# Optimization experiments

Hardware: AMD Instinct MI355X
Metric: run time of the kernel (lower is better)

Reference implementation:

```python
import jax, jax.numpy as jnp
import numpy as np

NEG_SLOPE = 0.01  # nn.LeakyReLU default

N = 100000
E = 1600000
D_IN = 128
D_OUT = 128


def setup_inputs() -> dict:
    key = jax.random.key(0)
    ks = jax.random.split(key, 8)
    features = jax.random.normal(ks[0], (N, D_IN), dtype=jnp.float32)
    adj_rows = jax.random.randint(ks[1], (E,), 0, N, dtype=jnp.int64)
    adj_cols = jax.random.randint(ks[2], (E,), 0, N, dtype=jnp.int64)
    adj_vals = jax.random.uniform(ks[3], (E,), dtype=jnp.float32)
    s1 = 1.0 / np.sqrt(D_IN)
    W1 = jax.random.uniform(ks[4], (D_IN, D_OUT), jnp.float32, -s1, s1)
    b1 = jax.random.uniform(ks[5], (D_OUT,), jnp.float32, -s1, s1)
    W2 = jax.random.uniform(ks[6], (D_IN, D_OUT), jnp.float32, -s1, s1)
    b2 = jax.random.uniform(ks[7], (D_OUT,), jnp.float32, -s1, s1)
    return {"features": features, "adj_rows": adj_rows, "adj_cols": adj_cols,
            "adj_vals": adj_vals, "W1": W1, "b1": b1, "W2": W2, "b2": b2}


def reference(features, adj_rows, adj_cols, adj_vals, W1, b1, W2, b2):
    # h_neigh = adj @ features  (COO SpMM via gather + segment_sum)
    msgs = adj_vals[:, None] * features[adj_cols]          # [E, D_IN]
    h_neigh = jax.ops.segment_sum(msgs, adj_rows, num_segments=features.shape[0])
    term1 = (features + h_neigh) @ W1 + b1                 # W1(features + h_neigh)
    term2 = (features * h_neigh) @ W2 + b2                 # W2(features * h_neigh)
    pre = term1 + term2
    return jnp.where(pre >= 0, pre, NEG_SLOPE * pre)       # leaky_relu
```

## Files before the change

### kernel.cpp

```cpp
#include <hip/hip_runtime.h>

#define D 128
#define BM 64

typedef short short8 __attribute__((ext_vector_type(8)));
typedef unsigned short ushort8_t __attribute__((ext_vector_type(8)));
typedef float f32x4 __attribute__((ext_vector_type(4)));

__device__ __forceinline__ unsigned short f2bf(float x) {
    unsigned u = __float_as_uint(x);
    unsigned r = (u + 0x7fffu + ((u >> 16) & 1u)) >> 16;
    return (unsigned short)r;
}
__device__ __forceinline__ float bf2f(unsigned short u) {
    return __uint_as_float(((unsigned)u) << 16);
}

__global__ __launch_bounds__(256) void prep_kernel(
    const float4* __restrict__ feat4, ushort4* __restrict__ fbf4, int nf4,
    const float* __restrict__ W1, const float* __restrict__ W2,
    unsigned short* __restrict__ WT,
    const int* __restrict__ rows, int* __restrict__ bcnt,
    int E, int nb, int epb)
{
    __shared__ int cnt[1024];
    const int t = threadIdx.x;
    const int b = blockIdx.x;
    for (int i = t; i < nb; i += 256) cnt[i] = 0;
    __syncthreads();

    int e0 = b * epb;
    int e1 = e0 + epb; if (e1 > E) e1 = E;
    for (int e = e0 + t; e < e1; e += 256) atomicAdd(&cnt[rows[e] >> 7], 1);

    for (int i = b * 256 + t; i < nf4; i += 256 * 256) {
        float4 v = feat4[i];
        fbf4[i] = make_ushort4(f2bf(v.x), f2bf(v.y), f2bf(v.z), f2bf(v.w));
    }

    if (b < 128) {
        int idx = b * 256 + t;
        int c = idx & 127;
        int k = idx >> 7;
        float w = (k < 128) ? W1[k * 128 + c] : W2[(k - 128) * 128 + c];
        WT[c * 256 + k] = f2bf(w);
    }

    __syncthreads();
    for (int i = t; i < nb; i += 256)
        if (cnt[i]) atomicAdd(&bcnt[i], cnt[i]);
}

__global__ __launch_bounds__(256) void fconv_kernel(
    const float4* __restrict__ feat4, ushort4* __restrict__ fbf4, int total)
{
    int i = blockIdx.x * 256 + threadIdx.x;
    if (i < total) {
        float4 v = feat4[i];
        fbf4[i] = make_ushort4(f2bf(v.x), f2bf(v.y), f2bf(v.z), f2bf(v.w));
    }
}

__global__ __launch_bounds__(256) void wconv_kernel(
    const float* __restrict__ W1, const float* __restrict__ W2,
    unsigned short* __restrict__ WT)
{
    int idx = blockIdx.x * 256 + threadIdx.x;
    int c = idx & 127;
    int k = idx >> 7;
    float w = (k < 128) ? W1[k * 128 + c] : W2[(k - 128) * 128 + c];
    WT[c * 256 + k] = f2bf(w);
}

__global__ __launch_bounds__(1024) void bucket_scan_kernel(
    const int* __restrict__ bcnt, int* __restrict__ bstart,
    int* __restrict__ bcur, int nb, int E)
{
    __shared__ int wsum[16];
    int tid = threadIdx.x, lane = tid & 63, wid = tid >> 6;
    int x = (tid < nb) ? bcnt[tid] : 0;
    int v = x;
    #pragma unroll
    for (int off = 1; off < 64; off <<= 1) {
        int y = __shfl_up(v, off, 64);
        if (lane >= off) v += y;
    }
    if (lane == 63) wsum[wid] = v;
    __syncthreads();
    if (wid == 0 && lane < 16) {
        int s = wsum[lane];
        #pragma unroll
        for (int off = 1; off < 16; off <<= 1) {
            int y = __shfl_up(s, off, 64);
            if (lane >= off) s += y;
        }
        wsum[lane] = s;
    }
    __syncthreads();
    int wexcl = wid ? wsum[wid - 1] : 0;
    int excl = wexcl + v - x;
    if (tid < nb) { bstart[tid] = excl; bcur[tid] = excl; }
    if (tid == 0) bstart[nb] = E;
}

__global__ __launch_bounds__(256) void bucket_scatter_kernel(
    const int* __restrict__ rows, const int* __restrict__ cols,
    const float* __restrict__ vals, int* __restrict__ bcur,
    uint2* __restrict__ bsedge, int E, int nb)
{
    __shared__ int cnt[1024];
    __shared__ int base[1024];
    int t = threadIdx.x;
    int e0 = blockIdx.x * 4096;
    for (int i = t; i < nb; i += 256) cnt[i] = 0;
    __syncthreads();
    #pragma unroll
    for (int q = 0; q < 16; ++q) {
        int e = e0 + t + q * 256;
        if (e < E) atomicAdd(&cnt[rows[e] >> 7], 1);
    }
    __syncthreads();
    for (int i = t; i < nb; i += 256) {
        int c = cnt[i];
        if (c) { base[i] = atomicAdd(&bcur[i], c); cnt[i] = 0; }
    }
    __syncthreads();
    #pragma unroll
    for (int q = 0; q < 16; ++q) {
        int e = e0 + t + q * 256;
        if (e < E) {
            int r = rows[e];
            int b = r >> 7;
            int pos = base[b] + atomicAdd(&cnt[b], 1);
            bsedge[pos] = make_uint2(((unsigned)(r & 127) << 17) | (unsigned)cols[e],
                                     __float_as_uint(vals[e]));
        }
    }
}

__global__ __launch_bounds__(256) void bucket_sort_kernel(
    const uint2* __restrict__ bsedge,
    const int* __restrict__ bstart,
    uint2* __restrict__ sedge,
    int* __restrict__ row_start,
    int N, int E)
{
    __shared__ int cnt[128];
    __shared__ int base[128];
    const int b = blockIdx.x;
    const int t = threadIdx.x;
    const int s = bstart[b], e = bstart[b + 1];
    if (t < 128) cnt[t] = 0;
    __syncthreads();
    for (int j = s + t; j < e; j += 256)
        atomicAdd(&cnt[bsedge[j].x >> 17], 1);
    __syncthreads();
    if (t < 64) {
        int c0 = cnt[2 * t], c1 = cnt[2 * t + 1];
        int pair = c0 + c1;
        int v = pair;
        #pragma unroll
        for (int off = 1; off < 64; off <<= 1) {
            int y = __shfl_up(v, off, 64);
            if (t >= off) v += y;
        }
        int excl = v - pair;
        base[2 * t]     = excl;
        base[2 * t + 1] = excl + c0;
        cnt[2 * t] = 0;
        cnt[2 * t + 1] = 0;
    }
    __syncthreads();
    const int r0 = b << 7;
    if (t < 128 && r0 + t < N) row_start[r0 + t] = s + base[t];
    if (b == 0 && t == 0) row_start[N] = E;
    for (int j = s + t; j < e; j += 256) {
        uint2 ed = bsedge[j];
        int rl = ed.x >> 17;
        int p = atomicAdd(&cnt[rl], 1);
        sedge[s + base[rl] + p] = make_uint2(ed.x & 0x1FFFFu, ed.y);
    }
}

__global__ __launch_bounds__(256) void spmm_ab_kernel(
    const ushort8_t* __restrict__ fbf8,
    const int* __restrict__ row_start,
    const uint2* __restrict__ sedge,
    unsigned char* __restrict__ ambf, int N)
{
    int t = blockIdx.x * 256 + threadIdx.x;
    int row  = t >> 5;
    int half = (t >> 4) & 1;
    int l    = t & 15;
    if (row >= N) return;

    int s = row_start[row];
    int e = row_start[row + 1];
    int mid = s + ((e - s + 1) >> 1);
    int j0 = half ? mid : s;
    int j1 = half ? e : mid;

    float acc[8] = {};
    int j = j0;
    for (; j + 3 < j1; j += 4) {
        uint2 e0 = sedge[j],     e1 = sedge[j + 1];
        uint2 e2 = sedge[j + 2], e3 = sedge[j + 3];
        ushort8_t f0 = fbf8[(size_t)e0.x * 16 + l];
        ushort8_t f1 = fbf8[(size_t)e1.x * 16 + l];
        ushort8_t f2 = fbf8[(size_t)e2.x * 16 + l];
        ushort8_t f3 = fbf8[(size_t)e3.x * 16 + l];
        float v0 = __uint_as_float(e0.y), v1 = __uint_as_float(e1.y);
        float v2 = __uint_as_float(e2.y), v3 = __uint_as_float(e3.y);
        #pragma unroll
        for (int q = 0; q < 8; ++q) {
            acc[q] = fmaf(v0, bf2f(f0[q]), acc[q]);
            acc[q] = fmaf(v1, bf2f(f1[q]), acc[q]);
            acc[q] = fmaf(v2, bf2f(f2[q]), acc[q]);
            acc[q] = fmaf(v3, bf2f(f3[q]), acc[q]);
        }
    }
    for (; j < j1; ++j) {
        uint2 e0 = sedge[j];
        float v = __uint_as_float(e0.y);
        ushort8_t f0 = fbf8[(size_t)e0.x * 16 + l];
        #pragma unroll
        for (int q = 0; q < 8; ++q) acc[q] = fmaf(v, bf2f(f0[q]), acc[q]);
    }

    #pragma unroll
    for (int q = 0; q < 8; ++q)
        acc[q] += __shfl_xor(acc[q], 16, 64);

    if (half == 0) {
        ushort8_t fown = fbf8[(size_t)row * 16 + l];
        ushort8_t av, mv;
        #pragma unroll
        for (int q = 0; q < 8; ++q) {
            float f = bf2f(fown[q]);
            av[q] = f2bf(f + acc[q]);
            mv[q] = f2bf(f * acc[q]);
        }
        int swz = (row & 7) << 4;
        unsigned char* rowp = ambf + (size_t)row * 512;
        *(ushort8_t*)(rowp + ((16 * l) ^ swz))       = av;
        *(ushort8_t*)(rowp + 256 + ((16 * l) ^ swz)) = mv;
    }
}

__global__ __launch_bounds__(256) void mfma_gemm2_kernel(
    const unsigned char* __restrict__ ambf,
    const unsigned short* __restrict__ WT,
    const float* __restrict__ b1, const float* __restrict__ b2,
    float* __restrict__ out, int N)
{
    __shared__ __align__(16) unsigned char am_raw[64 * 512];

    const int tid = threadIdx.x;
    const int block0 = blockIdx.x * BM;

    const short8* src = (const short8*)(ambf + (size_t)block0 * 512);
    short8* dst = (short8*)am_raw;
    #pragma unroll
    for (int it = 0; it < 8; ++it) {
        int idx = tid + it * 256;
        dst[idx] = src[idx];
    }
    __syncthreads();

    const int lane = tid & 63;
    const int w    = tid >> 6;
    const int wr   = w >> 1;
    const int wc   = w & 1;
    const int l15  = lane & 15;
    const int lk   = lane >> 4;
    const int rswz = (l15 & 7) << 4;

    f32x4 acc[2][4] = {};

    const char* WTc = (const char*)WT;
    const unsigned char* arow0 = am_raw + (wr * 32 + l15) * 512;
    const unsigned char* arow1 = arow0 + 16 * 512;

    #pragma unroll
    for (int ks = 0; ks < 8; ++ks) {
        int kbyte = ks * 64 + lk * 16;
        int akoff = kbyte ^ rswz;
        short8 a0 = *(const short8*)(arow0 + akoff);
        short8 a1 = *(const short8*)(arow1 + akoff);
        short8 bfr[4];
        #pragma unroll
        for (int nc = 0; nc < 4; ++nc) {
            int col = wc * 64 + nc * 16 + l15;
            bfr[nc] = *(const short8*)(WTc + col * 512 + kbyte);
        }
        #pragma unroll
        for (int nc = 0; nc < 4; ++nc) {
            acc[0][nc] = __builtin_amdgcn_mfma_f32_16x16x32_bf16(a0, bfr[nc], acc[0][nc], 0, 0, 0);
            acc[1][nc] = __builtin_amdgcn_mfma_f32_16x16x32_bf16(a1, bfr[nc], acc[1][nc], 0, 0, 0);
        }
    }

    #pragma unroll
    for (int nc = 0; nc < 4; ++nc) {
        int col = wc * 64 + nc * 16 + l15;
        float bias = b1[col] + b2[col];
        #pragma unroll
        for (int mr = 0; mr < 2; ++mr) {
            int rbase = block0 + wr * 32 + mr * 16 + lk * 4;
            #pragma unroll
            for (int r = 0; r < 4; ++r) {
                int row = rbase + r;
                if (row < N) {
                    float v = acc[mr][nc][r] + bias;
                    out[row * 128 + col] = (v >= 0.f) ? v : 0.01f * v;
                }
            }
        }
    }
}

__global__ __launch_bounds__(256) void hist_kernel(
    const int* __restrict__ rows, int* __restrict__ counts, int E)
{
    int e = blockIdx.x * 256 + threadIdx.x;
    if (e < E) atomicAdd(&counts[rows[e]], 1);
}

__global__ __launch_bounds__(256) void scan_pass1(
    const int* __restrict__ counts, int* __restrict__ btot, int N)
{
    int tid = threadIdx.x;
    int i = blockIdx.x * 1024 + tid * 4;
    int s = 0;
    if (i + 3 < N) {
        int4 v = *(const int4*)(counts + i);
        s = v.x + v.y + v.z + v.w;
    } else {
        for (int q = 0; q < 4; ++q) if (i + q < N) s += counts[i + q];
    }
    #pragma unroll
    for (int off = 32; off >= 1; off >>= 1) s += __shfl_down(s, off, 64);
    __shared__ int ws[4];
    if ((tid & 63) == 0) ws[tid >> 6] = s;
    __syncthreads();
    if (tid == 0) btot[blockIdx.x] = ws[0] + ws[1] + ws[2] + ws[3];
}

__global__ __launch_bounds__(1024) void scan_pass2(
    const int* __restrict__ btot, int* __restrict__ boff, int nb)
{
    __shared__ int wsum[16];
    int tid = threadIdx.x, lane = tid & 63, wid = tid >> 6;
    int x = (tid < nb) ? btot[tid] : 0;
    int v = x;
    #pragma unroll
    for (int off = 1; off < 64; off <<= 1) {
        int y = __shfl_up(v, off, 64);
        if (lane >= off) v += y;
    }
    if (lane == 63) wsum[wid] = v;
    __syncthreads();
    if (wid == 0 && lane < 16) {
        int s = wsum[lane];
        #pragma unroll
        for (int off = 1; off < 16; off <<= 1) {
            int y = __shfl_up(s, off, 64);
            if (lane >= off) s += y;
        }
        wsum[lane] = s;
    }
    __syncthreads();
    int wexcl = wid ? wsum[wid - 1] : 0;
    if (tid < nb) boff[tid] = wexcl + v - x;
}

__global__ __launch_bounds__(256) void scan_pass3(
    int* __restrict__ row_start, int* __restrict__ cursor,
    const int* __restrict__ boff, int N, int E)
{
    int tid = threadIdx.x;
    int base = blockIdx.x * 1024 + tid * 4;
    int c0 = 0, c1 = 0, c2 = 0, c3 = 0;
    if (base + 3 < N) {
        int4 v = *(const int4*)(row_start + base);
        c0 = v.x; c1 = v.y; c2 = v.z; c3 = v.w;
    } else {
        if (base + 0 < N) c0 = row_start[base + 0];
        if (base + 1 < N) c1 = row_start[base + 1];
        if (base + 2 < N) c2 = row_start[base + 2];
        if (base + 3 < N) c3 = row_start[base + 3];
    }
    int s0 = c0, s1 = s0 + c1, s2 = s1 + c2, s3 = s2 + c3;
    int lane = tid & 63, wid = tid >> 6;
    int v = s3;
    #pragma unroll
    for (int off = 1; off < 64; off <<= 1) {
        int y = __shfl_up(v, off, 64);
        if (lane >= off) v += y;
    }
    __shared__ int ws[4];
    if (lane == 63) ws[wid] = v;
    __syncthreads();
    int wexcl = 0;
    for (int q = 0; q < wid; ++q) wexcl += ws[q];
    int texcl = wexcl + (v - s3) + boff[blockIdx.x];
    int e0 = texcl, e1 = texcl + s0, e2 = texcl + s1, e3 = texcl + s2;
    if (base + 0 < N) { row_start[base + 0] = e0; cursor[base + 0] = e0; }
    if (base + 1 < N) { row_start[base + 1] = e1; cursor[base + 1] = e1; }
    if (base + 2 < N) { row_start[base + 2] = e2; cursor[base + 2] = e2; }
    if (base + 3 < N) { row_start[base + 3] = e3; cursor[base + 3] = e3; }
    if (blockIdx.x == 0 && tid == 0) row_start[N] = E;
}

__global__ __launch_bounds__(256) void scatter_sort_kernel(
    const int* __restrict__ rows, const int* __restrict__ cols,
    const float* __restrict__ vals, int* __restrict__ cursor,
    uint2* __restrict__ sedge, int E)
{
    int e = blockIdx.x * 256 + threadIdx.x;
    if (e < E) {
        int r = rows[e];
        int p = atomicAdd(&cursor[r], 1);
        sedge[p] = make_uint2((unsigned)cols[e], __float_as_uint(vals[e]));
    }
}

__global__ __launch_bounds__(256) void spmm_kernel(
    const float2* __restrict__ feat2,
    const int* __restrict__ row_start,
    const uint2* __restrict__ sedge,
    float2* __restrict__ h2, int N)
{
    int gw = (blockIdx.x * 256 + threadIdx.x) >> 6;
    int lane = threadIdx.x & 63;
    if (gw >= N) return;
    int s = row_start[gw];
    int e = row_start[gw + 1];
    float2 acc = make_float2(0.f, 0.f);
    int j = s;
    for (; j + 1 < e; j += 2) {
        uint2 e0 = sedge[j], e1 = sedge[j + 1];
        float v0 = __uint_as_float(e0.y), v1 = __uint_as_float(e1.y);
        float2 f0 = feat2[(size_t)e0.x * 64 + lane];
        float2 f1 = feat2[(size_t)e1.x * 64 + lane];
        acc.x = fmaf(v0, f0.x, acc.x);
        acc.y = fmaf(v0, f0.y, acc.y);
        acc.x = fmaf(v1, f1.x, acc.x);
        acc.y = fmaf(v1, f1.y, acc.y);
    }
    if (j < e) {
        uint2 e0 = sedge[j];
        float v = __uint_as_float(e0.y);
        float2 f = feat2[(size_t)e0.x * 64 + lane];
        acc.x = fmaf(v, f.x, acc.x);
        acc.y = fmaf(v, f.y, acc.y);
    }
    h2[(size_t)gw * 64 + lane] = acc;
}

__global__ __launch_bounds__(256) void mfma_gemm_kernel(
    const float4* __restrict__ feat4, const float4* __restrict__ h4,
    const unsigned short* __restrict__ WT,
    const float* __restrict__ b1, const float* __restrict__ b2,
    float* __restrict__ out, int N)
{
    __shared__ __align__(16) unsigned char am_raw[64 * 512];
    const int tid = threadIdx.x;
    const int block0 = blockIdx.x * BM;
    #pragma unroll
    for (int it = 0; it < 8; ++it) {
        int idx  = tid + it * 256;
        int node = idx >> 5;
        int p    = idx & 31;
        int g    = block0 + node;
        float4 fv = make_float4(0.f, 0.f, 0.f, 0.f);
        float4 hv = make_float4(0.f, 0.f, 0.f, 0.f);
        if (g < N) { fv = feat4[g * 32 + p]; hv = h4[g * 32 + p]; }
        ushort4 av = make_ushort4(f2bf(fv.x + hv.x), f2bf(fv.y + hv.y),
                                  f2bf(fv.z + hv.z), f2bf(fv.w + hv.w));
        ushort4 mv = make_ushort4(f2bf(fv.x * hv.x), f2bf(fv.y * hv.y),
                                  f2bf(fv.z * hv.z), f2bf(fv.w * hv.w));
        int swz = (node & 7) << 4;
        *(ushort4*)(am_raw + node * 512 + ((p * 8) ^ swz))       = av;
        *(ushort4*)(am_raw + node * 512 + ((256 + p * 8) ^ swz)) = mv;
    }
    __syncthreads();
    const int lane = tid & 63;
    const int w    = tid >> 6;
    const int wr   = w >> 1;
    const int wc   = w & 1;
    const int l15  = lane & 15;
    const int lk   = lane >> 4;
    const int rswz = (l15 & 7) << 4;
    f32x4 acc[2][4] = {};
    const char* WTc = (const char*)WT;
    const unsigned char* arow0 = am_raw + (wr * 32 + l15) * 512;
    const unsigned char* arow1 = arow0 + 16 * 512;
    #pragma unroll
    for (int ks = 0; ks < 8; ++ks) {
        int kbyte = ks * 64 + lk * 16;
        int akoff = kbyte ^ rswz;
        short8 a0 = *(const short8*)(arow0 + akoff);
        short8 a1 = *(const short8*)(arow1 + akoff);
        short8 bfr[4];
        #pragma unroll
        for (int nc = 0; nc < 4; ++nc) {
            int col = wc * 64 + nc * 16 + l15;
            bfr[nc] = *(const short8*)(WTc + col * 512 + kbyte);
        }
        #pragma unroll
        for (int nc = 0; nc < 4; ++nc) {
            acc[0][nc] = __builtin_amdgcn_mfma_f32_16x16x32_bf16(a0, bfr[nc], acc[0][nc], 0, 0, 0);
            acc[1][nc] = __builtin_amdgcn_mfma_f32_16x16x32_bf16(a1, bfr[nc], acc[1][nc], 0, 0, 0);
        }
    }
    #pragma unroll
    for (int nc = 0; nc < 4; ++nc) {
        int col = wc * 64 + nc * 16 + l15;
        float bias = b1[col] + b2[col];
        #pragma unroll
        for (int mr = 0; mr < 2; ++mr) {
            int rbase = block0 + wr * 32 + mr * 16 + lk * 4;
            #pragma unroll
            for (int r = 0; r < 4; ++r) {
                int row = rbase + r;
                if (row < N) {
                    float v = acc[mr][nc][r] + bias;
                    out[row * 128 + col] = (v >= 0.f) ? v : 0.01f * v;
                }
            }
        }
    }
}

__global__ __launch_bounds__(256) void edge_scatter_kernel(
    const float4* __restrict__ feat4, const int* __restrict__ rows,
    const int* __restrict__ cols, const float* __restrict__ vals,
    float* __restrict__ h, int E)
{
    int idx = blockIdx.x * 256 + threadIdx.x;
    if (idx >= E * 32) return;
    int e = idx >> 5;
    int p = idx & 31;
    int r = rows[e];
    int c = cols[e];
    float v = vals[e];
    float4 f = feat4[c * 32 + p];
    float* hr = h + (long long)r * D + p * 4;
    unsafeAtomicAdd(hr + 0, v * f.x);
    unsafeAtomicAdd(hr + 1, v * f.y);
    unsafeAtomicAdd(hr + 2, v * f.z);
    unsafeAtomicAdd(hr + 3, v * f.w);
}

__global__ __launch_bounds__(256) void fused_gemm_kernel(
    const float* __restrict__ feat, const float* __restrict__ h,
    const float* __restrict__ W1, const float* __restrict__ b1,
    const float* __restrict__ W2, const float* __restrict__ b2,
    float* __restrict__ out, int N)
{
    __shared__ float a_lds[BM][D];
    __shared__ float m_lds[BM][D];
    const int tid = threadIdx.x;
    const int block0 = blockIdx.x * BM;
    const float4* feat4 = (const float4*)feat;
    const float4* h4    = (const float4*)h;
    #pragma unroll
    for (int it = 0; it < 8; ++it) {
        int idx  = tid + it * 256;
        int node = idx >> 5;
        int p    = idx & 31;
        int gnode = block0 + node;
        float4 fv = make_float4(0.f, 0.f, 0.f, 0.f);
        float4 hv = make_float4(0.f, 0.f, 0.f, 0.f);
        if (gnode < N) { fv = feat4[gnode * 32 + p]; hv = h4[gnode * 32 + p]; }
        float4 av = make_float4(fv.x + hv.x, fv.y + hv.y, fv.z + hv.z, fv.w + hv.w);
        float4 mv = make_float4(fv.x * hv.x, fv.y * hv.y, fv.z * hv.z, fv.w * hv.w);
        *(float4*)&a_lds[node][p * 4] = av;
        *(float4*)&m_lds[node][p * 4] = mv;
    }
    __syncthreads();
    const int c = tid & 31;
    const int g = tid >> 5;
    float acc[8][4] = {};
    const float4* W1v = (const float4*)W1;
    const float4* W2v = (const float4*)W2;
    for (int k = 0; k < D; ++k) {
        float4 w1 = W1v[k * 32 + c];
        float4 w2 = W2v[k * 32 + c];
        #pragma unroll
        for (int t = 0; t < 8; ++t) {
            float av = a_lds[g + 8 * t][k];
            float mv = m_lds[g + 8 * t][k];
            acc[t][0] = fmaf(av, w1.x, fmaf(mv, w2.x, acc[t][0]));
            acc[t][1] = fmaf(av, w1.y, fmaf(mv, w2.y, acc[t][1]));
            acc[t][2] = fmaf(av, w1.z, fmaf(mv, w2.z, acc[t][2]));
            acc[t][3] = fmaf(av, w1.w, fmaf(mv, w2.w, acc[t][3]));
        }
    }
    float4 bb1 = ((const float4*)b1)[c];
    float4 bb2 = ((const float4*)b2)[c];
    const float bx = bb1.x + bb2.x, by = bb1.y + bb2.y;
    const float bz = bb1.z + bb2.z, bw = bb1.w + bb2.w;
    #pragma unroll
    for (int t = 0; t < 8; ++t) {
        int gnode = block0 + g + 8 * t;
        if (gnode >= N) continue;
        float4 o;
        o.x = acc[t][0] + bx; o.y = acc[t][1] + by;
        o.z = acc[t][2] + bz; o.w = acc[t][3] + bw;
        o.x = (o.x >= 0.f) ? o.x : 0.01f * o.x;
        o.y = (o.y >= 0.f) ? o.y : 0.01f * o.y;
        o.z = (o.z >= 0.f) ? o.z : 0.01f * o.z;
        o.w = (o.w >= 0.f) ? o.w : 0.01f * o.w;
        ((float4*)out)[gnode * 32 + c] = o;
    }
}

extern "C" void kernel_launch(void* const* d_in, const int* in_sizes, int n_in,
                              void* d_out, int out_size, void* d_ws, size_t ws_size,
                              hipStream_t stream) {
    const float* feat = (const float*)d_in[0];
    const int*   rows = (const int*)d_in[1];
    const int*   cols = (const int*)d_in[2];
    const float* vals = (const float*)d_in[3];
    const float* W1   = (const float*)d_in[4];
    const float* b1   = (const float*)d_in[5];
    const float* W2   = (const float*)d_in[6];
    const float* b2   = (const float*)d_in[7];

    const int N = in_sizes[0] / D;
    const int E = in_sizes[1];
    float* out = (float*)d_out;

    const int NBK  = (N + 127) >> 7;
    const int Npad = NBK << 7;

    size_t off = 0;
    unsigned char* ambf = (unsigned char*)d_ws;                    off += (size_t)Npad * 512;
    unsigned short* featbf = (unsigned short*)((char*)d_ws + off); off += (size_t)N * D * 2;
    off = (off + 15) & ~(size_t)15;
    uint2* sedge = (uint2*)((char*)d_ws + off);                    off += (size_t)E * 8;
    unsigned short* WT = (unsigned short*)((char*)d_ws + off);     off += 128 * 256 * 2;
    int* row_start = (int*)((char*)d_ws + off);                    off += (size_t)(N + 1) * 4;
    off = (off + 15) & ~(size_t)15;
    uint2* bsedge = (uint2*)((char*)d_ws + off);                   off += (size_t)E * 8;
    int* bcnt   = (int*)((char*)d_ws + off);                       off += (size_t)NBK * 4;
    int* bstart = (int*)((char*)d_ws + off);                       off += (size_t)(NBK + 1) * 4;
    int* bcur   = (int*)((char*)d_ws + off);                       off += (size_t)NBK * 4;
    size_t need1a = off;

    if (ws_size >= need1a && NBK <= 1024 && N <= (1 << 17)) {
        hipMemsetAsync(bcnt, 0, (size_t)NBK * sizeof(int), stream);
        int epb = (E + 255) / 256;
        prep_kernel<<<256, 256, 0, stream>>>(
            (const float4*)feat, (ushort4*)featbf, N * 32,
            W1, W2, WT, rows, bcnt, E, NBK, epb);
        bucket_scan_kernel<<<1, 1024, 0, stream>>>(bcnt, bstart, bcur, NBK, E);
        bucket_scatter_kernel<<<(E + 4095) / 4096, 256, 0, stream>>>(
            rows, cols, vals, bcur, bsedge, E, NBK);
        bucket_sort_kernel<<<NBK, 256, 0, stream>>>(
            bsedge, bstart, sedge, row_start, N, E);
        spmm_ab_kernel<<<((size_t)N * 32 + 255) / 256, 256, 0, stream>>>(
            (const ushort8_t*)featbf, row_start, sedge, ambf, N);
        mfma_gemm2_kernel<<<(N + BM - 1) / BM, 256, 0, stream>>>(
            ambf, WT, b1, b2, out, N);
        return;
    }

    const int NB = (N + 1023) / 1024;
    off = 0;
    ambf = (unsigned char*)d_ws;                                   off += (size_t)Npad * 512;
    featbf = (unsigned short*)((char*)d_ws + off);                 off += (size_t)N * D * 2;
    off = (off + 15) & ~(size_t)15;
    sedge = (uint2*)((char*)d_ws + off);                           off += (size_t)E * 8;
    WT = (unsigned short*)((char*)d_ws + off);                     off += 128 * 256 * 2;
    row_start = (int*)((char*)d_ws + off);                         off += (size_t)(N + 1) * 4;
    off = (off + 15) & ~(size_t)15;
    int* cursor = (int*)((char*)d_ws + off);                       off += (size_t)N * 4;
    int* btot = (int*)((char*)d_ws + off);                         off += (size_t)NB * 4;
    int* boff = (int*)((char*)d_ws + off);                         off += (size_t)NB * 4;
    size_t need1b = off;

    if (ws_size >= need1b && NB <= 1024) {
        hipMemsetAsync(row_start, 0, (size_t)(N + 1) * sizeof(int), stream);
        fconv_kernel<<<(N * 32 + 255) / 256, 256, 0, stream>>>(
            (const float4*)feat, (ushort4*)featbf, N * 32);
        wconv_kernel<<<128, 256, 0, stream>>>(W1, W2, WT);
        hist_kernel<<<(E + 255) / 256, 256, 0, stream>>>(rows, row_start, E);
        scan_pass1<<<NB, 256, 0, stream>>>(row_start, btot, N);
        scan_pass2<<<1, 1024, 0, stream>>>(btot, boff, NB);
        scan_pass3<<<NB, 256, 0, stream>>>(row_start, cursor, boff, N, E);
        scatter_sort_kernel<<<(E + 255) / 256, 256, 0, stream>>>(
            rows, cols, vals, cursor, sedge, E);
        spmm_ab_kernel<<<((size_t)N * 32 + 255) / 256, 256, 0, stream>>>(
            (const ushort8_t*)featbf, row_start, sedge, ambf, N);
        mfma_gemm2_kernel<<<(N + BM - 1) / BM, 256, 0, stream>>>(
            ambf, WT, b1, b2, out, N);
        return;
    }

    off = 0;
    float* h = (float*)d_ws;                           off += (size_t)N * D * 4;
    int* row_start2 = (int*)((char*)d_ws + off);       off += (size_t)(N + 1) * 4;
    int* cursor2    = (int*)((char*)d_ws + off);       off += (size_t)N * 4;
    off = (off + 15) & ~(size_t)15;
    uint2* sedge2   = (uint2*)((char*)d_ws + off);     off += (size_t)E * 8;
    off = (off + 15) & ~(size_t)15;
    unsigned short* WT2 = (unsigned short*)((char*)d_ws + off); off += 128 * 256 * 2;
    int* btot2 = (int*)((char*)d_ws + off);            off += (size_t)NB * 4;
    int* boff2 = (int*)((char*)d_ws + off);            off += (size_t)NB * 4;
    size_t need2 = off;

    if (ws_size >= need2 && NB <= 1024) {
        hipMemsetAsync(row_start2, 0, (size_t)(N + 1) * sizeof(int), stream);
        wconv_kernel<<<128, 256, 0, stream>>>(W1, W2, WT2);
        hist_kernel<<<(E + 255) / 256, 256, 0, stream>>>(rows, row_start2, E);
        scan_pass1<<<NB, 256, 0, stream>>>(row_start2, btot2, N);
        scan_pass2<<<1, 1024, 0, stream>>>(btot2, boff2, NB);
        scan_pass3<<<NB, 256, 0, stream>>>(row_start2, cursor2, boff2, N, E);
        scatter_sort_kernel<<<(E + 255) / 256, 256, 0, stream>>>(
            rows, cols, vals, cursor2, sedge2, E);
        spmm_kernel<<<(N * 64 + 255) / 256, 256, 0, stream>>>(
            (const float2*)feat, row_start2, sedge2, (float2*)h, N);
        mfma_gemm_kernel<<<(N + BM - 1) / BM, 256, 0, stream>>>(
            (const float4*)feat, (const float4*)h, WT2, b1, b2, out, N);
        return;
    }

    size_t hbytes = (size_t)N * D * sizeof(float);
    float* hh = (ws_size >= hbytes) ? (float*)d_ws : out;
    hipMemsetAsync(hh, 0, hbytes, stream);
    edge_scatter_kernel<<<((size_t)E * 32 + 255) / 256, 256, 0, stream>>>(
        (const float4*)feat, rows, cols, vals, hh, E);
    fused_gemm_kernel<<<(N + BM - 1) / BM, 256, 0, stream>>>(
        feat, hh, W1, b1, W2, b2, out, N);
}
```

Baseline: 192.3 us.

## Fuse SpMM aggregation with MFMA GEMM epilogue via shared-memory tiles

Replaces the separate SpMM kernel (which wrote bf16 [f+h, f*h] rows to global workspace) and the follow-up MFMA GEMM kernel with one kernel per 16-row tile. Each block gathers neighbours, builds the combined A rows in swizzled LDS, then runs a 16x128 MFMA product with bias and leaky ReLU. This removes the global write and re-read of the intermediate buffer and one launch. In exchange, each block re-reads the full 128x256 weight matrix from global/L2 for only 16 rows, and the GEMM tile is small.

```diff
diff --git a/kernel.cpp b/kernel.cpp
--- a/kernel.cpp
+++ b/kernel.cpp
@@ -179,6 +179,112 @@
         int rl = ed.x >> 17;
         int p = atomicAdd(&cnt[rl], 1);
         sedge[s + base[rl] + p] = make_uint2(ed.x & 0x1FFFFu, ed.y);
+    }
+}
+
+__global__ __launch_bounds__(512) void spmm_gemm16_kernel(
+    const ushort8_t* __restrict__ fbf8,
+    const int* __restrict__ row_start,
+    const uint2* __restrict__ sedge,
+    const unsigned short* __restrict__ WT,
+    const float* __restrict__ b1, const float* __restrict__ b2,
+    float* __restrict__ out, int N)
+{
+    __shared__ __align__(16) unsigned char am_raw[16 * 512];
+
+    const int tid = threadIdx.x;
+    const int block0 = blockIdx.x * 16;
+    const int rq   = tid >> 5;
+    const int half = (tid >> 4) & 1;
+    const int l    = tid & 15;
+
+    int row = block0 + rq;
+    float acc[8] = {};
+    if (row < N) {
+        int s = row_start[row];
+        int e = row_start[row + 1];
+        int mid = s + ((e - s + 1) >> 1);
+        int j0 = half ? mid : s;
+        int j1 = half ? e : mid;
+        int j = j0;
+        for (; j + 3 < j1; j += 4) {
+            uint2 e0 = sedge[j],     e1 = sedge[j + 1];
+            uint2 e2 = sedge[j + 2], e3 = sedge[j + 3];
+            ushort8_t f0 = fbf8[(size_t)e0.x * 16 + l];
+            ushort8_t f1 = fbf8[(size_t)e1.x * 16 + l];
+            ushort8_t f2 = fbf8[(size_t)e2.x * 16 + l];
+            ushort8_t f3 = fbf8[(size_t)e3.x * 16 + l];
+            float v0 = __uint_as_float(e0.y), v1 = __uint_as_float(e1.y);
+            float v2 = __uint_as_float(e2.y), v3 = __uint_as_float(e3.y);
+            #pragma unroll
+            for (int q = 0; q < 8; ++q) {
+                acc[q] = fmaf(v0, bf2f(f0[q]), acc[q]);
+                acc[q] = fmaf(v1, bf2f(f1[q]), acc[q]);
+                acc[q] = fmaf(v2, bf2f(f2[q]), acc[q]);
+                acc[q] = fmaf(v3, bf2f(f3[q]), acc[q]);
+            }
+        }
+        for (; j < j1; ++j) {
+            uint2 e0 = sedge[j];
+            float v = __uint_as_float(e0.y);
+            ushort8_t f0 = fbf8[(size_t)e0.x * 16 + l];
+            #pragma unroll
+            for (int q = 0; q < 8; ++q) acc[q] = fmaf(v, bf2f(f0[q]), acc[q]);
+        }
+    }
+
+    #pragma unroll
+    for (int q = 0; q < 8; ++q)
+        acc[q] += __shfl_xor(acc[q], 16, 64);
+
+    if (half == 0) {
+        float f[8] = {};
+        if (row < N) {
+            ushort8_t fown = fbf8[(size_t)row * 16 + l];
+            #pragma unroll
+            for (int q = 0; q < 8; ++q) f[q] = bf2f(fown[q]);
+        }
+        ushort8_t av, mv;
+        #pragma unroll
+        for (int q = 0; q < 8; ++q) {
+            av[q] = f2bf(f[q] + acc[q]);
+            mv[q] = f2bf(f[q] * acc[q]);
+        }
+        int swz = (rq & 7) << 4;
+        unsigned char* rowp = am_raw + rq * 512;
+        *(ushort8_t*)(rowp + ((16 * l) ^ swz))       = av;
+        *(ushort8_t*)(rowp + 256 + ((16 * l) ^ swz)) = mv;
+    }
+    __syncthreads();
+
+    const int lane = tid & 63;
+    const int w    = tid >> 6;
+    const int l15  = lane & 15;
+    const int lk   = lane >> 4;
+    const int rswz = (l15 & 7) << 4;
+
+    f32x4 gacc = {};
+    const char* WTc = (const char*)WT;
+    const unsigned char* arow = am_raw + l15 * 512;
+    const int col = w * 16 + l15;
+
+    #pragma unroll
+    for (int ks = 0; ks < 8; ++ks) {
+        int kbyte = ks * 64 + lk * 16;
+        short8 a = *(const short8*)(arow + (kbyte ^ rswz));
+        short8 b = *(const short8*)(WTc + col * 512 + kbyte);
+        gacc = __builtin_amdgcn_mfma_f32_16x16x32_bf16(a, b, gacc, 0, 0, 0);
+    }
+
+    float bias = b1[col] + b2[col];
+    int rbase = block0 + lk * 4;
+    #pragma unroll
+    for (int r = 0; r < 4; ++r) {
+        int orow = rbase + r;
+        if (orow < N) {
+            float v = gacc[r] + bias;
+            out[orow * 128 + col] = (v >= 0.f) ? v : 0.01f * v;
+        }
     }
 }
 
@@ -637,8 +743,7 @@
     const int Npad = NBK << 7;
 
     size_t off = 0;
-    unsigned char* ambf = (unsigned char*)d_ws;                    off += (size_t)Npad * 512;
-    unsigned short* featbf = (unsigned short*)((char*)d_ws + off); off += (size_t)N * D * 2;
+    unsigned short* featbf = (unsigned short*)d_ws;                off += (size_t)N * D * 2;
     off = (off + 15) & ~(size_t)15;
     uint2* sedge = (uint2*)((char*)d_ws + off);                    off += (size_t)E * 8;
     unsigned short* WT = (unsigned short*)((char*)d_ws + off);     off += 128 * 256 * 2;
@@ -661,16 +766,14 @@
             rows, cols, vals, bcur, bsedge, E, NBK);
         bucket_sort_kernel<<<NBK, 256, 0, stream>>>(
             bsedge, bstart, sedge, row_start, N, E);
-        spmm_ab_kernel<<<((size_t)N * 32 + 255) / 256, 256, 0, stream>>>(
-            (const ushort8_t*)featbf, row_start, sedge, ambf, N);
-        mfma_gemm2_kernel<<<(N + BM - 1) / BM, 256, 0, stream>>>(
-            ambf, WT, b1, b2, out, N);
+        spmm_gemm16_kernel<<<(N + 15) / 16, 512, 0, stream>>>(
+            (const ushort8_t*)featbf, row_start, sedge, WT, b1, b2, out, N);
         return;
     }
 
     const int NB = (N + 1023) / 1024;
     off = 0;
-    ambf = (unsigned char*)d_ws;                                   off += (size_t)Npad * 512;
+    unsigned char* ambf = (unsigned char*)d_ws;                    off += (size_t)Npad * 512;
     featbf = (unsigned short*)((char*)d_ws + off);                 off += (size_t)N * D * 2;
     off = (off + 15) & ~(size_t)15;
     sedge = (uint2*)((char*)d_ws + off);                           off += (size_t)E * 8;
```

Result: faster. 187.9 us (-2.3%).

## Fuse per-bucket row sort into SpMM kernel using shared-memory edge staging

Applied to the files above, without the earlier changes.

Replaces the separate bucket_sort pass (which wrote a fully row-sorted edge array and row_start to global memory) with a fused kernel. Each 128-row bucket counts and scans its rows and scatters its edges into LDS (up to 3072 edges), then does the gather-accumulate and writes the bf16 add/mul operands directly. This removes one kernel launch and a global write plus read of the sorted edge list. In exchange each bucket uses one 512-thread block with serialized rows per 16-lane group, which may lower parallelism, and it falls back to a slow scan over all edges if a bucket overflows CAP.

```diff
diff --git a/kernel.cpp b/kernel.cpp
--- a/kernel.cpp
+++ b/kernel.cpp
@@ -2,6 +2,7 @@
 
 #define D 128
 #define BM 64
+#define CAP 3072
 
 typedef short short8 __attribute__((ext_vector_type(8)));
 typedef unsigned short ushort8_t __attribute__((ext_vector_type(8)));
@@ -134,6 +135,206 @@
             int pos = base[b] + atomicAdd(&cnt[b], 1);
             bsedge[pos] = make_uint2(((unsigned)(r & 127) << 17) | (unsigned)cols[e],
                                      __float_as_uint(vals[e]));
+        }
+    }
+}
+
+__global__ __launch_bounds__(512) void spmm_sort_ab_kernel(
+    const ushort8_t* __restrict__ fbf8,
+    const int* __restrict__ bstart,
+    const uint2* __restrict__ bsedge,
+    unsigned char* __restrict__ ambf, int N)
+{
+    __shared__ uint2 sL[CAP];
+    __shared__ int cnt[128];
+    __shared__ int base[129];
+
+    const int t = threadIdx.x;
+    const int b = blockIdx.x;
+    const int s = bstart[b], e = bstart[b + 1];
+    const int M = e - s;
+
+    if (t < 128) cnt[t] = 0;
+    __syncthreads();
+    for (int j = s + t; j < e; j += 512)
+        atomicAdd(&cnt[bsedge[j].x >> 17], 1);
+    __syncthreads();
+    if (t < 64) {
+        int c0 = cnt[2 * t], c1 = cnt[2 * t + 1];
+        int pair = c0 + c1;
+        int v = pair;
+        #pragma unroll
+        for (int off = 1; off < 64; off <<= 1) {
+            int y = __shfl_up(v, off, 64);
+            if (t >= off) v += y;
+        }
+        int excl = v - pair;
+        base[2 * t]     = excl;
+        base[2 * t + 1] = excl + c0;
+        if (t == 63) base[128] = excl + pair;
+        cnt[2 * t] = 0;
+        cnt[2 * t + 1] = 0;
+    }
+    __syncthreads();
+
+    const int g = t >> 4;
+    const int l = t & 15;
+
+    if (M <= CAP) {
+        for (int j = s + t; j < e; j += 512) {
+            uint2 ed = bsedge[j];
+            int rl = ed.x >> 17;
+            int p = atomicAdd(&cnt[rl], 1);
+            sL[base[rl] + p] = make_uint2(ed.x & 0x1FFFFu, ed.y);
+        }
+        __syncthreads();
+
+        #pragma unroll
+        for (int rr = 0; rr < 4; ++rr) {
+            int rl = g + rr * 32;
+            int row = (b << 7) + rl;
+            if (row >= N) continue;
+            int j  = base[rl];
+            int j1 = base[rl + 1];
+            float acc[8] = {};
+            for (; j + 3 < j1; j += 4) {
+                uint2 e0 = sL[j],     e1 = sL[j + 1];
+                uint2 e2 = sL[j + 2], e3 = sL[j + 3];
+                ushort8_t f0 = fbf8[(size_t)e0.x * 16 + l];
+                ushort8_t f1 = fbf8[(size_t)e1.x * 16 + l];
+                ushort8_t f2 = fbf8[(size_t)e2.x * 16 + l];
+                ushort8_t f3 = fbf8[(size_t)e3.x * 16 + l];
+                float v0 = __uint_as_float(e0.y), v1 = __uint_as_float(e1.y);
+                float v2 = __uint_as_float(e2.y), v3 = __uint_as_float(e3.y);
+                #pragma unroll
+                for (int q = 0; q < 8; ++q) {
+                    acc[q] = fmaf(v0, bf2f(f0[q]), acc[q]);
+                    acc[q] = fmaf(v1, bf2f(f1[q]), acc[q]);
+                    acc[q] = fmaf(v2, bf2f(f2[q]), acc[q]);
+                    acc[q] = fmaf(v3, bf2f(f3[q]), acc[q]);
+                }
+            }
+            for (; j < j1; ++j) {
+                uint2 e0 = sL[j];
+                float v = __uint_as_float(e0.y);
+                ushort8_t f0 = fbf8[(size_t)e0.x * 16 + l];
+                #pragma unroll
+                for (int q = 0; q < 8; ++q) acc[q] = fmaf(v, bf2f(f0[q]), acc[q]);
+            }
+
+            ushort8_t fown = fbf8[(size_t)row * 16 + l];
+            ushort8_t av, mv;
+            #pragma unroll
+            for (int q = 0; q < 8; ++q) {
+                float f = bf2f(fown[q]);
+                av[q] = f2bf(f + acc[q]);
+                mv[q] = f2bf(f * acc[q]);
+            }
+            int swz = (row & 7) << 4;
+            unsigned char* rowp = ambf + (size_t)row * 512;
+            *(ushort8_t*)(rowp + ((16 * l) ^ swz))       = av;
+            *(ushort8_t*)(rowp + 256 + ((16 * l) ^ swz)) = mv;
+        }
+    } else {
+        #pragma unroll
+        for (int rr = 0; rr < 4; ++rr) {
+            int rl = g + rr * 32;
+            int row = (b << 7) + rl;
+            if (row >= N) continue;
+            float acc[8] = {};
+            for (int j = s; j < e; ++j) {
+                uint2 ed = bsedge[j];
+                if ((int)(ed.x >> 17) == rl) {
+                    float v = __uint_as_float(ed.y);
+                    ushort8_t f0 = fbf8[(size_t)(ed.x & 0x1FFFFu) * 16 + l];
+                    #pragma unroll
+                    for (int q = 0; q < 8; ++q) acc[q] = fmaf(v, bf2f(f0[q]), acc[q]);
+                }
+            }
+            ushort8_t fown = fbf8[(size_t)row * 16 + l];
+            ushort8_t av, mv;
+            #pragma unroll
+            for (int q = 0; q < 8; ++q) {
+                float f = bf2f(fown[q]);
+                av[q] = f2bf(f + acc[q]);
+                mv[q] = f2bf(f * acc[q]);
+            }
+            int swz = (row & 7) << 4;
+            unsigned char* rowp = ambf + (size_t)row * 512;
+            *(ushort8_t*)(rowp + ((16 * l) ^ swz))       = av;
+            *(ushort8_t*)(rowp + 256 + ((16 * l) ^ swz)) = mv;
+        }
+    }
+}
+
+__global__ __launch_bounds__(256) void mfma_gemm2_kernel(
+    const unsigned char* __restrict__ ambf,
+    const unsigned short* __restrict__ WT,
+    const float* __restrict__ b1, const float* __restrict__ b2,
+    float* __restrict__ out, int N)
+{
+    __shared__ __align__(16) unsigned char am_raw[64 * 512];
+
+    const int tid = threadIdx.x;
+    const int block0 = blockIdx.x * BM;
+
+    const short8* src = (const short8*)(ambf + (size_t)block0 * 512);
+    short8* dst = (short8*)am_raw;
+    #pragma unroll
+    for (int it = 0; it < 8; ++it) {
+        int idx = tid + it * 256;
+        dst[idx] = src[idx];
+    }
+    __syncthreads();
+
+    const int lane = tid & 63;
+    const int w    = tid >> 6;
+    const int wr   = w >> 1;
+    const int wc   = w & 1;
+    const int l15  = lane & 15;
+    const int lk   = lane >> 4;
+    const int rswz = (l15 & 7) << 4;
+
+    f32x4 acc[2][4] = {};
+
+    const char* WTc = (const char*)WT;
+    const unsigned char* arow0 = am_raw + (wr * 32 + l15) * 512;
+    const unsigned char* arow1 = arow0 + 16 * 512;
+
+    #pragma unroll
+    for (int ks = 0; ks < 8; ++ks) {
+        int kbyte = ks * 64 + lk * 16;
+        int akoff = kbyte ^ rswz;
+        short8 a0 = *(const short8*)(arow0 + akoff);
+        short8 a1 = *(const short8*)(arow1 + akoff);
+        short8 bfr[4];
+        #pragma unroll
+        for (int nc = 0; nc < 4; ++nc) {
+            int col = wc * 64 + nc * 16 + l15;
+            bfr[nc] = *(const short8*)(WTc + col * 512 + kbyte);
+        }
+        #pragma unroll
+        for (int nc = 0; nc < 4; ++nc) {
+            acc[0][nc] = __builtin_amdgcn_mfma_f32_16x16x32_bf16(a0, bfr[nc], acc[0][nc], 0, 0, 0);
+            acc[1][nc] = __builtin_amdgcn_mfma_f32_16x16x32_bf16(a1, bfr[nc], acc[1][nc], 0, 0, 0);
+        }
+    }
+
+    #pragma unroll
+    for (int nc = 0; nc < 4; ++nc) {
+        int col = wc * 64 + nc * 16 + l15;
+        float bias = b1[col] + b2[col];
+        #pragma unroll
+        for (int mr = 0; mr < 2; ++mr) {
+            int rbase = block0 + wr * 32 + mr * 16 + lk * 4;
+            #pragma unroll
+            for (int r = 0; r < 4; ++r) {
+                int row = rbase + r;
+                if (row < N) {
+                    float v = acc[mr][nc][r] + bias;
+                    out[row * 128 + col] = (v >= 0.f) ? v : 0.01f * v;
+                }
+            }
         }
     }
 }
@@ -244,78 +445,6 @@
         unsigned char* rowp = ambf + (size_t)row * 512;
         *(ushort8_t*)(rowp + ((16 * l) ^ swz))       = av;
         *(ushort8_t*)(rowp + 256 + ((16 * l) ^ swz)) = mv;
-    }
-}
-
-__global__ __launch_bounds__(256) void mfma_gemm2_kernel(
-    const unsigned char* __restrict__ ambf,
-    const unsigned short* __restrict__ WT,
-    const float* __restrict__ b1, const float* __restrict__ b2,
-    float* __restrict__ out, int N)
-{
-    __shared__ __align__(16) unsigned char am_raw[64 * 512];
-
-    const int tid = threadIdx.x;
-    const int block0 = blockIdx.x * BM;
-
-    const short8* src = (const short8*)(ambf + (size_t)block0 * 512);
-    short8* dst = (short8*)am_raw;
-    #pragma unroll
-    for (int it = 0; it < 8; ++it) {
-        int idx = tid + it * 256;
-        dst[idx] = src[idx];
-    }
-    __syncthreads();
-
-    const int lane = tid & 63;
-    const int w    = tid >> 6;
-    const int wr   = w >> 1;
-    const int wc   = w & 1;
-    const int l15  = lane & 15;
-    const int lk   = lane >> 4;
-    const int rswz = (l15 & 7) << 4;
-
-    f32x4 acc[2][4] = {};
-
-    const char* WTc = (const char*)WT;
-    const unsigned char* arow0 = am_raw + (wr * 32 + l15) * 512;
-    const unsigned char* arow1 = arow0 + 16 * 512;
-
-    #pragma unroll
-    for (int ks = 0; ks < 8; ++ks) {
-        int kbyte = ks * 64 + lk * 16;
-        int akoff = kbyte ^ rswz;
-        short8 a0 = *(const short8*)(arow0 + akoff);
-        short8 a1 = *(const short8*)(arow1 + akoff);
-        short8 bfr[4];
-        #pragma unroll
-        for (int nc = 0; nc < 4; ++nc) {
-            int col = wc * 64 + nc * 16 + l15;
-            bfr[nc] = *(const short8*)(WTc + col * 512 + kbyte);
-        }
-        #pragma unroll
-        for (int nc = 0; nc < 4; ++nc) {
-            acc[0][nc] = __builtin_amdgcn_mfma_f32_16x16x32_bf16(a0, bfr[nc], acc[0][nc], 0, 0, 0);
-            acc[1][nc] = __builtin_amdgcn_mfma_f32_16x16x32_bf16(a1, bfr[nc], acc[1][nc], 0, 0, 0);
-        }
-    }
-
-    #pragma unroll
-    for (int nc = 0; nc < 4; ++nc) {
-        int col = wc * 64 + nc * 16 + l15;
-        float bias = b1[col] + b2[col];
-        #pragma unroll
-        for (int mr = 0; mr < 2; ++mr) {
-            int rbase = block0 + wr * 32 + mr * 16 + lk * 4;
-            #pragma unroll
-            for (int r = 0; r < 4; ++r) {
-                int row = rbase + r;
-                if (row < N) {
-                    float v = acc[mr][nc][r] + bias;
-                    out[row * 128 + col] = (v >= 0.f) ? v : 0.01f * v;
-                }
-            }
-        }
     }
 }
 
@@ -640,9 +769,7 @@
     unsigned char* ambf = (unsigned char*)d_ws;                    off += (size_t)Npad * 512;
     unsigned short* featbf = (unsigned short*)((char*)d_ws + off); off += (size_t)N * D * 2;
     off = (off + 15) & ~(size_t)15;
-    uint2* sedge = (uint2*)((char*)d_ws + off);                    off += (size_t)E * 8;
     unsigned short* WT = (unsigned short*)((char*)d_ws + off);     off += 128 * 256 * 2;
-    int* row_start = (int*)((char*)d_ws + off);                    off += (size_t)(N + 1) * 4;
     off = (off + 15) & ~(size_t)15;
     uint2* bsedge = (uint2*)((char*)d_ws + off);                   off += (size_t)E * 8;
     int* bcnt   = (int*)((char*)d_ws + off);                       off += (size_t)NBK * 4;
@@ -651,6 +778,36 @@
     size_t need1a = off;
 
     if (ws_size >= need1a && NBK <= 1024 && N <= (1 << 17)) {
+        hipMemsetAsync(bcnt, 0, (size_t)NBK * sizeof(int), stream);
+        int epb = (E + 255) / 256;
+        prep_kernel<<<256, 256, 0, stream>>>(
+            (const float4*)feat, (ushort4*)featbf, N * 32,
+            W1, W2, WT, rows, bcnt, E, NBK, epb);
+        bucket_scan_kernel<<<1, 1024, 0, stream>>>(bcnt, bstart, bcur, NBK, E);
+        bucket_scatter_kernel<<<(E + 4095) / 4096, 256, 0, stream>>>(
+            rows, cols, vals, bcur, bsedge, E, NBK);
+        spmm_sort_ab_kernel<<<NBK, 512, 0, stream>>>(
+            (const ushort8_t*)featbf, bstart, bsedge, ambf, N);
+        mfma_gemm2_kernel<<<(N + BM - 1) / BM, 256, 0, stream>>>(
+            ambf, WT, b1, b2, out, N);
+        return;
+    }
+
+    off = 0;
+    ambf = (unsigned char*)d_ws;                                   off += (size_t)Npad * 512;
+    featbf = (unsigned short*)((char*)d_ws + off);                 off += (size_t)N * D * 2;
+    off = (off + 15) & ~(size_t)15;
+    uint2* sedge = (uint2*)((char*)d_ws + off);                    off += (size_t)E * 8;
+    WT = (unsigned short*)((char*)d_ws + off);                     off += 128 * 256 * 2;
+    int* row_start = (int*)((char*)d_ws + off);                    off += (size_t)(N + 1) * 4;
+    off = (off + 15) & ~(size_t)15;
+    bsedge = (uint2*)((char*)d_ws + off);                          off += (size_t)E * 8;
+    bcnt   = (int*)((char*)d_ws + off);                            off += (size_t)NBK * 4;
+    bstart = (int*)((char*)d_ws + off);                            off += (size_t)(NBK + 1) * 4;
+    bcur   = (int*)((char*)d_ws + off);                            off += (size_t)NBK * 4;
+    size_t need1b = off;
+
+    if (ws_size >= need1b && NBK <= 1024 && N <= (1 << 17)) {
         hipMemsetAsync(bcnt, 0, (size_t)NBK * sizeof(int), stream);
         int epb = (E + 255) / 256;
         prep_kernel<<<256, 256, 0, stream>>>(
@@ -670,37 +827,6 @@
 
     const int NB = (N + 1023) / 1024;
     off = 0;
-    ambf = (unsigned char*)d_ws;                                   off += (size_t)Npad * 512;
-    featbf = (unsigned short*)((char*)d_ws + off);                 off += (size_t)N * D * 2;
-    off = (off + 15) & ~(size_t)15;
-    sedge = (uint2*)((char*)d_ws + off);                           off += (size_t)E * 8;
-    WT = (unsigned short*)((char*)d_ws + off);                     off += 128 * 256 * 2;
-    row_start = (int*)((char*)d_ws + off);                         off += (size_t)(N + 1) * 4;
-    off = (off + 15) & ~(size_t)15;
-    int* cursor = (int*)((char*)d_ws + off);                       off += (size_t)N * 4;
-    int* btot = (int*)((char*)d_ws + off);                         off += (size_t)NB * 4;
-    int* boff = (int*)((char*)d_ws + off);                         off += (size_t)NB * 4;
-    size_t need1b = off;
-
-    if (ws_size >= need1b && NB <= 1024) {
-        hipMemsetAsync(row_start, 0, (size_t)(N + 1) * sizeof(int), stream);
-        fconv_kernel<<<(N * 32 + 255) / 256, 256, 0, stream>>>(
-            (const float4*)feat, (ushort4*)featbf, N * 32);
-        wconv_kernel<<<128, 256, 0, stream>>>(W1, W2, WT);
-        hist_kernel<<<(E + 255) / 256, 256, 0, stream>>>(rows, row_start, E);
-        scan_pass1<<<NB, 256, 0, stream>>>(row_start, btot, N);
-        scan_pass2<<<1, 1024, 0, stream>>>(btot, boff, NB);
-        scan_pass3<<<NB, 256, 0, stream>>>(row_start, cursor, boff, N, E);
-        scatter_sort_kernel<<<(E + 255) / 256, 256, 0, stream>>>(
-            rows, cols, vals, cursor, sedge, E);
-        spmm_ab_kernel<<<((size_t)N * 32 + 255) / 256, 256, 0, stream>>>(
-            (const ushort8_t*)featbf, row_start, sedge, ambf, N);
-        mfma_gemm2_kernel<<<(N + BM - 1) / BM, 256, 0, stream>>>(
-            ambf, WT, b1, b2, out, N);
-        return;
-    }
-
-    off = 0;
     float* h = (float*)d_ws;                           off += (size_t)N * D * 4;
     int* row_start2 = (int*)((char*)d_ws + off);       off += (size_t)(N + 1) * 4;
     int* cursor2    = (int*)((char*)d_ws + off);       off += (size_t)N * 4;
```

Result: faster. 185.0 us (-3.8%).
